# Performance work log

Hardware: AMD Instinct MI355X
Metric: run time of the kernel (lower is better)

## Reference

```python
import jax, jax.numpy as jnp
import numpy as np

HIDDEN = 4096
N_HEADS = 32
HEAD_DIM = HIDDEN // N_HEADS
B = 8
S = 1024
N = B * S


def _build_cos_sin(max_pos, head_dim):
    inv_freq = 1.0 / (10000.0 ** (np.arange(0, head_dim, 2, dtype=np.float32) / head_dim))
    t = np.arange(max_pos, dtype=np.float32)
    freqs = np.outer(t, inv_freq)                 # [max_pos, head_dim/2]
    emb = np.concatenate([freqs, freqs], axis=-1)  # [max_pos, head_dim]
    return jnp.asarray(np.cos(emb)), jnp.asarray(np.sin(emb))


def setup_inputs() -> dict:
    key = jax.random.key(0)
    ks = jax.random.split(key, 5)
    cos, sin = _build_cos_sin(S, HEAD_DIM)
    scale = 0.02
    inp = {
        "cos": cos,
        "sin": sin,
        "nz_hidden_states": jax.random.normal(ks[0], (N, HIDDEN), jnp.float32),
        "nz_position_ids": jnp.tile(jnp.arange(S, dtype=jnp.int32), B),
        "cu_seqlens": jnp.arange(B + 1, dtype=jnp.int32) * S,
        "max_seqlen": S,
        "Wq": jax.random.normal(ks[1], (HIDDEN, HIDDEN), jnp.float32) * scale,
        "Wk": jax.random.normal(ks[2], (HIDDEN, HIDDEN), jnp.float32) * scale,
        "Wv": jax.random.normal(ks[3], (HIDDEN, HIDDEN), jnp.float32) * scale,
        "Wo": jax.random.normal(ks[4], (HIDDEN, HIDDEN), jnp.float32) * scale,
    }
    return inp


def _rotate_half(x):
    x1, x2 = jnp.split(x, 2, axis=-1)
    return jnp.concatenate([-x2, x1], axis=-1)


def reference(cos, sin, nz_hidden_states, nz_position_ids, cu_seqlens, max_seqlen, Wq, Wk, Wv, Wo):
    n_tok = nz_hidden_states.shape[0]
    b = cu_seqlens.shape[0] - 1
    s = n_tok // b  # equal-length packing
    h, d = N_HEADS, HEAD_DIM

    q = (nz_hidden_states @ Wq.T).reshape(n_tok, h, d)
    k = (nz_hidden_states @ Wk.T).reshape(n_tok, h, d)
    v = (nz_hidden_states @ Wv.T).reshape(n_tok, h, d)

    # RoPE: cos/sin gathered per token, broadcast over heads
    c = cos[nz_position_ids][:, None, :]  # [N,1,D]
    sn = sin[nz_position_ids][:, None, :]
    q = q * c + _rotate_half(q) * sn
    k = k * c + _rotate_half(k) * sn

    # Varlen causal attention (equal-length segments -> batch reshape)
    qb = q.reshape(b, s, h, d)
    kb = k.reshape(b, s, h, d)
    vb = v.reshape(b, s, h, d)
    scores = jnp.einsum('bqhd,bkhd->bhqk', qb, kb) / jnp.sqrt(jnp.float32(d))
    causal = jnp.tril(jnp.ones((s, s), dtype=bool))
    scores = jnp.where(causal, scores, jnp.finfo(scores.dtype).min)
    probs = jax.nn.softmax(scores, axis=-1)
    out = jnp.einsum('bhqk,bkhd->bqhd', probs, vb).reshape(n_tok, h * d)
    return out @ Wo.T
```

## Files before the change

kernel.cpp:

```cpp
#include <hip/hip_runtime.h>
#include <hip/hip_bf16.h>

#define NTOK 8192
#define HID 4096
#define NHEADS 32
#define HDIM 128
#define SEQ 1024
#define NSTEP (HID / 32)

typedef float f32x4 __attribute__((ext_vector_type(4)));
typedef short bf16x8 __attribute__((ext_vector_type(8)));

__device__ __forceinline__ ushort f2bf(float f) {
  union { float f; unsigned u; } x;
  x.f = f;
  unsigned r = x.u + 0x7fffu + ((x.u >> 16) & 1u);
  return (ushort)(r >> 16);
}
__device__ __forceinline__ float bf2f(ushort h) {
  union { unsigned u; float f; } x;
  x.u = ((unsigned)h) << 16;
  return x.f;
}

__global__ __launch_bounds__(256) void cvt_bf16_kernel(const float4* __restrict__ in,
                                                       ushort4* __restrict__ out, int n4) {
  int i = blockIdx.x * 256 + threadIdx.x;
  if (i < n4) {
    float4 v = in[i];
    ushort4 o;
    o.x = f2bf(v.x); o.y = f2bf(v.y); o.z = f2bf(v.z); o.w = f2bf(v.w);
    out[i] = o;
  }
}


__device__ __forceinline__ void gload16(const void* g, void* l) {
  __builtin_amdgcn_global_load_lds(
      (const __attribute__((address_space(1))) unsigned int*)g,
      (__attribute__((address_space(3))) unsigned int*)l, 16, 0, 0);
}

__device__ __forceinline__ void stage32(const ushort* gA, const ushort* gB,
                                        int rowA0, int rowB0, int k0,
                                        ushort* ldsA, ushort* ldsB, int tid) {
  const int wid = tid >> 6, lane = tid & 63;
#pragma unroll
  for (int q = 0; q < 2; ++q) {
    int wuni = q * 8192 + wid * 1024;
    int off = wuni + lane * 16;
    int row = off >> 6;
    int kb = (off ^ (((row >> 1) & 3) << 4)) & 63;
    gload16(gA + (size_t)(rowA0 + row) * HID + k0 + (kb >> 1), (char*)ldsA + wuni);
    gload16(gB + (size_t)(rowB0 + row) * HID + k0 + (kb >> 1), (char*)ldsB + wuni);
  }
}

__device__ __forceinline__ void load_frags(const ushort* sA, const ushort* sB,
                                           int wm, int wn, int l15, int l4, int swzr,
                                           bf16x8 af[8], bf16x8 bfr[4]) {
  const char* cA = (const char*)sA;
  const char* cB = (const char*)sB;
#pragma unroll
  for (int ii = 0; ii < 8; ++ii) {
    int L = (wm * 128 + ii * 16 + l15) * 64 + l4 * 16;
    af[ii] = *(const bf16x8*)(cA + (L ^ swzr));
  }
#pragma unroll
  for (int jj = 0; jj < 4; ++jj) {
    int L = (wn * 64 + jj * 16 + l15) * 64 + l4 * 16;
    bfr[jj] = *(const bf16x8*)(cB + (L ^ swzr));
  }
}

#define MFMA_CLUSTER()                                                         \
  do {                                                                         \
    asm volatile("s_waitcnt lgkmcnt(0)" ::: "memory");                         \
    __builtin_amdgcn_sched_barrier(0);                                         \
    __builtin_amdgcn_s_setprio(1);                                             \
    _Pragma("unroll") for (int ii = 0; ii < 8; ++ii)                           \
        _Pragma("unroll") for (int jj = 0; jj < 4; ++jj)                       \
            acc[ii][jj] = __builtin_amdgcn_mfma_f32_16x16x32_bf16(             \
                af[ii], bfr[jj], acc[ii][jj], 0, 0, 0);                        \
    __builtin_amdgcn_s_setprio(0);                                             \
  } while (0)

template <bool OUTF32>
__global__ __launch_bounds__(512, 2) void gemm256_kernel(
    const ushort* __restrict__ Abf,
    const ushort* __restrict__ B0, const ushort* __restrict__ B1,
    const ushort* __restrict__ B2,
    void* __restrict__ O0, void* __restrict__ O1, void* __restrict__ O2,
    int NTALL) {
  __shared__ __align__(16) ushort ringA[4][8192];
  __shared__ __align__(16) ushort ringB[4][8192];

  const int tid = threadIdx.x;
  const int l = tid & 63, wid = tid >> 6;
  const int wm = wid >> 2, wn = wid & 3;
  const int l15 = l & 15, l4 = l >> 4;
  const int swzr = ((l15 >> 1) & 3) << 4;

  const int nwg = gridDim.x;
  const int cpx = nwg >> 3;
  const int bid = blockIdx.x;
  const int lgid = (bid & 7) * cpx + (bid >> 3);
  const int bandw = NTALL << 3;
  const int band = lgid / bandw, rem = lgid % bandw;
  const int nt = rem >> 3;
  const int mt = (band << 3) + (rem & 7);
  const int m0 = mt * 256;
  const int sel = nt >> 4;
  const int n0 = (nt & 15) * 256;
  const ushort* Bp = (sel == 0) ? B0 : ((sel == 1) ? B1 : B2);
  void* Op = (sel == 0) ? O0 : ((sel == 1) ? O1 : O2);

  f32x4 acc[8][4];
  const f32x4 zero = {0.f, 0.f, 0.f, 0.f};
#pragma unroll
  for (int i = 0; i < 8; ++i)
#pragma unroll
    for (int j = 0; j < 4; ++j) acc[i][j] = zero;

  stage32(Abf, Bp, m0, n0, 0, ringA[0], ringB[0], tid);
  stage32(Abf, Bp, m0, n0, 32, ringA[1], ringB[1], tid);
  asm volatile("s_waitcnt vmcnt(4)" ::: "memory");
  __builtin_amdgcn_s_barrier();

  bf16x8 af[8], bfr[4];
#pragma unroll 4
  for (int t = 0; t < NSTEP - 2; ++t) {
    const int slot = t & 3;
    load_frags(ringA[slot], ringB[slot], wm, wn, l15, l4, swzr, af, bfr);
    stage32(Abf, Bp, m0, n0, (t + 2) * 32, ringA[(t + 2) & 3], ringB[(t + 2) & 3], tid);
    MFMA_CLUSTER();
    asm volatile("s_waitcnt vmcnt(4)" ::: "memory");
    __builtin_amdgcn_s_barrier();
  }
  load_frags(ringA[(NSTEP - 2) & 3], ringB[(NSTEP - 2) & 3], wm, wn, l15, l4, swzr, af, bfr);
  MFMA_CLUSTER();
  asm volatile("s_waitcnt vmcnt(0)" ::: "memory");
  __builtin_amdgcn_s_barrier();
  load_frags(ringA[(NSTEP - 1) & 3], ringB[(NSTEP - 1) & 3], wm, wn, l15, l4, swzr, af, bfr);
  MFMA_CLUSTER();

#pragma unroll
  for (int i = 0; i < 8; ++i) {
    const int row = m0 + wm * 128 + i * 16 + l4 * 4;
#pragma unroll
    for (int j = 0; j < 4; ++j) {
      const int col = n0 + wn * 64 + j * 16 + l15;
#pragma unroll
      for (int r = 0; r < 4; ++r) {
        float v = acc[i][j][r];
        if constexpr (OUTF32)
          ((float*)Op)[(size_t)(row + r) * HID + col] = v;
        else
          ((ushort*)Op)[(size_t)(row + r) * HID + col] = f2bf(v);
      }
    }
  }
}

template <bool ISBF>
__device__ __forceinline__ void stage_tile(ushort* lds, const void* gp, int row0, int k0, int tid) {
  if constexpr (ISBF) {
    const ushort* g = (const ushort*)gp;
#pragma unroll
    for (int i = 0; i < 2; ++i) {
      int row = (tid >> 2) + i * 64;
      int gr = tid & 3;
      bf16x8 v = *(const bf16x8*)(g + (size_t)(row0 + row) * HID + k0 + gr * 8);
      int gs = gr ^ ((row >> 1) & 3);
      *(bf16x8*)((char*)lds + row * 64 + gs * 16) = v;
    }
  } else {
    const float* g = (const float*)gp;
    int row = tid >> 1;
    const float* rp = g + (size_t)(row0 + row) * HID + k0;
#pragma unroll
    for (int i = 0; i < 2; ++i) {
      int gr = (tid & 1) * 2 + i;
      float4 a = *(const float4*)(rp + gr * 8);
      float4 b = *(const float4*)(rp + gr * 8 + 4);
      bf16x8 v;
      v[0] = (short)f2bf(a.x); v[1] = (short)f2bf(a.y);
      v[2] = (short)f2bf(a.z); v[3] = (short)f2bf(a.w);
      v[4] = (short)f2bf(b.x); v[5] = (short)f2bf(b.y);
      v[6] = (short)f2bf(b.z); v[7] = (short)f2bf(b.w);
      int gs = gr ^ ((row >> 1) & 3);
      *(bf16x8*)((char*)lds + row * 64 + gs * 16) = v;
    }
  }
}

template <bool ABF, bool BBF, bool OUTF32>
__global__ __launch_bounds__(256) void gemm_bt_kernel(
    const void* __restrict__ Ap,
    const void* __restrict__ B0, const void* __restrict__ B1, const void* __restrict__ B2,
    void* __restrict__ O0, void* __restrict__ O1, void* __restrict__ O2,
    int ntiles_per_w) {
  __shared__ __align__(16) ushort lA[128 * 32];
  __shared__ __align__(16) ushort lB[128 * 32];
  const int tid = threadIdx.x;
  const int l = tid & 63, wid = tid >> 6;
  const int wm = wid >> 1, wn = wid & 1;
  const int l15 = l & 15, l4 = l >> 4;
  const int mt0 = blockIdx.y * 128;
  const int ntile = blockIdx.x;
  const int sel = ntile / ntiles_per_w;
  const int nt0 = (ntile % ntiles_per_w) * 128;
  const void* Bp = (sel == 0) ? B0 : ((sel == 1) ? B1 : B2);
  void* Op = (sel == 0) ? O0 : ((sel == 1) ? O1 : O2);

  const f32x4 zero = {0.f, 0.f, 0.f, 0.f};
  f32x4 acc[4][4];
#pragma unroll
  for (int i = 0; i < 4; ++i)
#pragma unroll
    for (int j = 0; j < 4; ++j) acc[i][j] = zero;

  for (int k0 = 0; k0 < HID; k0 += 32) {
    stage_tile<ABF>(lA, Ap, mt0, k0, tid);
    stage_tile<BBF>(lB, Bp, nt0, k0, tid);
    __syncthreads();
    bf16x8 af[4], bfr[4];
#pragma unroll
    for (int i = 0; i < 4; ++i) {
      int rowa = wm * 64 + i * 16 + l15;
      int ga = l4 ^ ((rowa >> 1) & 3);
      af[i] = *(const bf16x8*)((const char*)lA + rowa * 64 + ga * 16);
      int rowb = wn * 64 + i * 16 + l15;
      int gb = l4 ^ ((rowb >> 1) & 3);
      bfr[i] = *(const bf16x8*)((const char*)lB + rowb * 64 + gb * 16);
    }
#pragma unroll
    for (int i = 0; i < 4; ++i)
#pragma unroll
      for (int j = 0; j < 4; ++j)
        acc[i][j] = __builtin_amdgcn_mfma_f32_16x16x32_bf16(af[i], bfr[j], acc[i][j], 0, 0, 0);
    __syncthreads();
  }

#pragma unroll
  for (int i = 0; i < 4; ++i) {
#pragma unroll
    for (int j = 0; j < 4; ++j) {
      int row = mt0 + wm * 64 + i * 16 + l4 * 4;
      int col = nt0 + wn * 64 + j * 16 + l15;
#pragma unroll
      for (int r = 0; r < 4; ++r) {
        float v = acc[i][j][r];
        if constexpr (OUTF32)
          ((float*)Op)[(size_t)(row + r) * HID + col] = v;
        else
          ((ushort*)Op)[(size_t)(row + r) * HID + col] = f2bf(v);
      }
    }
  }
}

__global__ __launch_bounds__(256) void rope_kernel(
    ushort* __restrict__ q, ushort* __restrict__ k,
    const float* __restrict__ cosT, const float* __restrict__ sinT,
    const int* __restrict__ pos) {
  int idx = blockIdx.x * 256 + threadIdx.x;
  int token = idx >> 8;
  int head = (idx >> 3) & 31;
  int c = idx & 7;
  int p = pos[token];
  size_t base = (size_t)token * HID + head * HDIM + c * 8;
  bf16x8 ql = *(bf16x8*)(q + base);
  bf16x8 qh = *(bf16x8*)(q + base + 64);
  bf16x8 kl = *(bf16x8*)(k + base);
  bf16x8 kh = *(bf16x8*)(k + base + 64);
  float4 c0 = *(const float4*)(cosT + (size_t)p * HDIM + c * 8);
  float4 c1 = *(const float4*)(cosT + (size_t)p * HDIM + c * 8 + 4);
  float4 s0 = *(const float4*)(sinT + (size_t)p * HDIM + c * 8);
  float4 s1 = *(const float4*)(sinT + (size_t)p * HDIM + c * 8 + 4);
  float cs[8] = {c0.x, c0.y, c0.z, c0.w, c1.x, c1.y, c1.z, c1.w};
  float sn[8] = {s0.x, s0.y, s0.z, s0.w, s1.x, s1.y, s1.z, s1.w};
  const float qsc = 0.08838834764831845f;
  bf16x8 qlo, qho, klo, kho;
#pragma unroll
  for (int j = 0; j < 8; ++j) {
    float qlf = bf2f((ushort)ql[j]), qhf = bf2f((ushort)qh[j]);
    float klf = bf2f((ushort)kl[j]), khf = bf2f((ushort)kh[j]);
    qlo[j] = (short)f2bf((qlf * cs[j] - qhf * sn[j]) * qsc);
    qho[j] = (short)f2bf((qhf * cs[j] + qlf * sn[j]) * qsc);
    klo[j] = (short)f2bf(klf * cs[j] - khf * sn[j]);
    kho[j] = (short)f2bf(khf * cs[j] + klf * sn[j]);
  }
  *(bf16x8*)(q + base) = qlo;
  *(bf16x8*)(q + base + 64) = qho;
  *(bf16x8*)(k + base) = klo;
  *(bf16x8*)(k + base + 64) = kho;
}

__global__ __launch_bounds__(256) void attn_kernel(
    const ushort* __restrict__ qb, const ushort* __restrict__ kb,
    const ushort* __restrict__ vb, ushort* __restrict__ ob) {
  __shared__ __align__(16) ushort lK[32 * 128];
  __shared__ __align__(16) ushort lVT[128 * 32];
  __shared__ __align__(16) ushort lP[4][16 * 32];

  const int tid = threadIdx.x;
  const int l = tid & 63, wid = tid >> 6;
  const int l15 = l & 15, l4 = l >> 4;
  const int q0 = blockIdx.x * 64;
  const int h = blockIdx.y;
  const size_t seqbase = (size_t)blockIdx.z * SEQ;

  bf16x8 qf[4];
  {
    const ushort* qp = qb + (seqbase + q0 + wid * 16 + l15) * HID + h * HDIM + l4 * 8;
#pragma unroll
    for (int kk = 0; kk < 4; ++kk) qf[kk] = *(const bf16x8*)(qp + kk * 32);
  }

  const f32x4 zero = {0.f, 0.f, 0.f, 0.f};
  f32x4 oacc[8];
#pragma unroll
  for (int t = 0; t < 8; ++t) oacc[t] = zero;
  float mrow[4] = {-3e38f, -3e38f, -3e38f, -3e38f};
  float lrow[4] = {0.f, 0.f, 0.f, 0.f};

  const int ntile = q0 / 32 + 2;
  for (int kt = 0; kt < ntile; ++kt) {
    const int k0 = kt * 32;
    {
      int r = tid >> 3;
      const ushort* kp = kb + (seqbase + k0 + r) * HID + h * HDIM;
#pragma unroll
      for (int i = 0; i < 2; ++i) {
        int g = (tid & 7) * 2 + i;
        bf16x8 kv = *(const bf16x8*)(kp + g * 8);
        int gs = g ^ (r & 7);
        *(bf16x8*)((char*)lK + r * 256 + gs * 16) = kv;
      }
    }
    {
      int d = tid & 127;
      int j0 = (tid >> 7) * 16;
      const ushort* vp = vb + (seqbase + k0 + j0) * HID + h * HDIM + d;
      ushort tmp[16];
#pragma unroll
      for (int j = 0; j < 16; ++j) tmp[j] = vp[(size_t)j * HID];
#pragma unroll
      for (int i = 0; i < 2; ++i) {
        bf16x8 vv;
#pragma unroll
        for (int jj = 0; jj < 8; ++jj) vv[jj] = (short)tmp[i * 8 + jj];
        int g = (j0 >> 3) + i;
        int gs = g ^ ((d >> 1) & 3);
        *(bf16x8*)((char*)lVT + d * 64 + gs * 16) = vv;
      }
    }
    __syncthreads();

    f32x4 s[2];
#pragma unroll
    for (int hf = 0; hf < 2; ++hf) {
      f32x4 c = zero;
      int row = hf * 16 + l15;
#pragma unroll
      for (int kk = 0; kk < 4; ++kk) {
        int gs = (kk * 4 + l4) ^ (row & 7);
        bf16x8 kf = *(const bf16x8*)((const char*)lK + row * 256 + gs * 16);
        c = __builtin_amdgcn_mfma_f32_16x16x32_bf16(qf[kk], kf, c, 0, 0, 0);
      }
      s[hf] = c;
    }

    const int qrow = q0 + wid * 16 + l4 * 4;
#pragma unroll
    for (int r = 0; r < 4; ++r) {
      float s0 = (k0 + l15 <= qrow + r) ? s[0][r] : -1e30f;
      float s1 = (k0 + 16 + l15 <= qrow + r) ? s[1][r] : -1e30f;
      float tmax = fmaxf(s0, s1);
#pragma unroll
      for (int off = 8; off; off >>= 1) tmax = fmaxf(tmax, __shfl_xor(tmax, off));
      float newm = fmaxf(mrow[r], tmax);
      float sc = __expf(mrow[r] - newm);
      float p0 = __expf(s0 - newm);
      float p1 = __expf(s1 - newm);
      float rs = p0 + p1;
#pragma unroll
      for (int off = 8; off; off >>= 1) rs += __shfl_xor(rs, off);
      lrow[r] = lrow[r] * sc + rs;
      mrow[r] = newm;
#pragma unroll
      for (int t = 0; t < 8; ++t) oacc[t][r] *= sc;
      lP[wid][(l4 * 4 + r) * 32 + l15] = f2bf(p0);
      lP[wid][(l4 * 4 + r) * 32 + 16 + l15] = f2bf(p1);
    }
    asm volatile("s_waitcnt lgkmcnt(0)" ::: "memory");
    __builtin_amdgcn_sched_barrier(0);

    bf16x8 pf = *(const bf16x8*)((const char*)&lP[wid][0] + l15 * 64 + l4 * 16);
#pragma unroll
    for (int t = 0; t < 8; ++t) {
      int d = t * 16 + l15;
      int gs = l4 ^ ((d >> 1) & 3);
      bf16x8 vf = *(const bf16x8*)((const char*)lVT + d * 64 + gs * 16);
      oacc[t] = __builtin_amdgcn_mfma_f32_16x16x32_bf16(pf, vf, oacc[t], 0, 0, 0);
    }
    __syncthreads();
  }

#pragma unroll
  for (int r = 0; r < 4; ++r) {
    float inv = 1.0f / lrow[r];
    ushort* op = ob + (seqbase + q0 + wid * 16 + l4 * 4 + r) * HID + h * HDIM + l15;
#pragma unroll
    for (int t = 0; t < 8; ++t) op[t * 16] = f2bf(oacc[t][r] * inv);
  }
}

extern "C" void kernel_launch(void* const* d_in, const int* in_sizes, int n_in,
                              void* d_out, int out_size, void* d_ws, size_t ws_size,
                              hipStream_t stream) {
  const float* cosT = (const float*)d_in[0];
  const float* sinT = (const float*)d_in[1];
  const float* X    = (const float*)d_in[2];
  const int*   pos  = (const int*)d_in[3];
  const float* Wq = (const float*)d_in[6];
  const float* Wk = (const float*)d_in[7];
  const float* Wv = (const float*)d_in[8];
  const float* Wo = (const float*)d_in[9];
  float* out = (float*)d_out;

  char* ws = (char*)d_ws;
  const size_t QKVB = (size_t)NTOK * HID * 2;
  const size_t WB = (size_t)HID * HID * 2;
  const size_t XB = QKVB;
  ushort* qbuf = (ushort*)(ws);
  ushort* kbuf = (ushort*)(ws + QKVB);
  ushort* vbuf = (ushort*)(ws + 2 * QKVB);

  dim3 blk(256);
  const int n4x = NTOK * HID / 4;
  const int n4w = HID * HID / 4;

  const bool fast = ws_size >= 3 * QKVB + XB + 4 * WB;
  const bool mid = !fast && ws_size >= 3 * QKVB + 2 * WB &&
                   (size_t)out_size * 4 >= XB + 2 * WB;

  if (fast || mid) {
    ushort *xb, *wqb, *wkb, *wvb, *wob;
    if (fast) {
      xb  = (ushort*)(ws + 3 * QKVB);
      wqb = (ushort*)(ws + 3 * QKVB + XB);
      wkb = (ushort*)(ws + 3 * QKVB + XB + WB);
      wvb = (ushort*)(ws + 3 * QKVB + XB + 2 * WB);
      wob = (ushort*)(ws + 3 * QKVB + XB + 3 * WB);
    } else {
      xb  = (ushort*)d_out;
      wqb = (ushort*)((char*)d_out + XB);
      wkb = (ushort*)((char*)d_out + XB + WB);
      wvb = (ushort*)(ws + 3 * QKVB);
      wob = (ushort*)(ws + 3 * QKVB + WB);
    }
    cvt_bf16_kernel<<<n4x / 256, blk, 0, stream>>>((const float4*)X, (ushort4*)xb, n4x);
    cvt_bf16_kernel<<<n4w / 256, blk, 0, stream>>>((const float4*)Wq, (ushort4*)wqb, n4w);
    cvt_bf16_kernel<<<n4w / 256, blk, 0, stream>>>((const float4*)Wk, (ushort4*)wkb, n4w);
    cvt_bf16_kernel<<<n4w / 256, blk, 0, stream>>>((const float4*)Wv, (ushort4*)wvb, n4w);
    cvt_bf16_kernel<<<n4w / 256, blk, 0, stream>>>((const float4*)Wo, (ushort4*)wob, n4w);
    gemm256_kernel<false><<<dim3(32 * 48), dim3(512), 0, stream>>>(
        xb, wqb, wkb, wvb, qbuf, kbuf, vbuf, 48);
    rope_kernel<<<NTOK * NHEADS * 8 / 256, blk, 0, stream>>>(qbuf, kbuf, cosT, sinT, pos);
    attn_kernel<<<dim3(16, 32, 8), blk, 0, stream>>>(qbuf, kbuf, vbuf, qbuf);
    gemm256_kernel<true><<<dim3(32 * 16), dim3(512), 0, stream>>>(
        qbuf, wob, wob, wob, out, out, out, 16);
  } else {
    gemm_bt_kernel<false, false, false><<<dim3(96, 64), blk, 0, stream>>>(
        X, Wq, Wk, Wv, qbuf, kbuf, vbuf, 32);
    rope_kernel<<<NTOK * NHEADS * 8 / 256, blk, 0, stream>>>(qbuf, kbuf, cosT, sinT, pos);
    attn_kernel<<<dim3(16, 32, 8), blk, 0, stream>>>(qbuf, kbuf, vbuf, qbuf);
    gemm_bt_kernel<true, false, true><<<dim3(32, 64), blk, 0, stream>>>(
        qbuf, Wo, Wo, Wo, out, out, out, 32);
  }
}
```

Before: 1.565 ms.

## Double-buffer register fragments and deepen LDS prefetch in GEMM main loop

The GEMM main loop now keeps two sets of register fragments. The LDS fragments for step t+1 are loaded while the MFMAs for step t run, which removes the lgkmcnt(0) wait and sched_barrier that came before each MFMA cluster. Global staging now runs three steps ahead instead of two in the 4-slot ring, and the loop is manually unrolled by four with a hand-written tail. This adds register pressure from the doubled fragment arrays at launch_bounds(512,2), so spills are a risk. The ring-slot reuse and its synchronization are also tighter, because slot t+3 is overwritten while slot t+1 is being read.

```diff
diff --git a/kernel.cpp b/kernel.cpp
--- a/kernel.cpp
+++ b/kernel.cpp
@@ -73,16 +73,22 @@
   }
 }
 
-#define MFMA_CLUSTER()                                                         \
+#define GSTEP(CURA, CURB, NXTA, NXTB, T, DO_STAGE, VMC)                        \
   do {                                                                         \
-    asm volatile("s_waitcnt lgkmcnt(0)" ::: "memory");                         \
-    __builtin_amdgcn_sched_barrier(0);                                         \
     __builtin_amdgcn_s_setprio(1);                                             \
     _Pragma("unroll") for (int ii = 0; ii < 8; ++ii)                           \
         _Pragma("unroll") for (int jj = 0; jj < 4; ++jj)                       \
             acc[ii][jj] = __builtin_amdgcn_mfma_f32_16x16x32_bf16(             \
-                af[ii], bfr[jj], acc[ii][jj], 0, 0, 0);                        \
+                CURA[ii], CURB[jj], acc[ii][jj], 0, 0, 0);                     \
     __builtin_amdgcn_s_setprio(0);                                             \
+    load_frags(ringA[((T) + 1) & 3], ringB[((T) + 1) & 3], wm, wn, l15, l4,    \
+               swzr, NXTA, NXTB);                                              \
+    if (DO_STAGE)                                                              \
+      stage32(Abf, Bp, m0, n0, ((T) + 3) * 32, ringA[((T) + 3) & 3],           \
+              ringB[((T) + 3) & 3], tid);                                      \
+    if ((VMC) == 4) asm volatile("s_waitcnt vmcnt(4)" ::: "memory");           \
+    else if ((VMC) == 0) asm volatile("s_waitcnt vmcnt(0)" ::: "memory");      \
+    __builtin_amdgcn_s_barrier();                                              \
   } while (0)
 
 template <bool OUTF32>
@@ -124,25 +130,43 @@
 
   stage32(Abf, Bp, m0, n0, 0, ringA[0], ringB[0], tid);
   stage32(Abf, Bp, m0, n0, 32, ringA[1], ringB[1], tid);
+  stage32(Abf, Bp, m0, n0, 64, ringA[2], ringB[2], tid);
   asm volatile("s_waitcnt vmcnt(4)" ::: "memory");
   __builtin_amdgcn_s_barrier();
 
-  bf16x8 af[8], bfr[4];
-#pragma unroll 4
-  for (int t = 0; t < NSTEP - 2; ++t) {
-    const int slot = t & 3;
-    load_frags(ringA[slot], ringB[slot], wm, wn, l15, l4, swzr, af, bfr);
-    stage32(Abf, Bp, m0, n0, (t + 2) * 32, ringA[(t + 2) & 3], ringB[(t + 2) & 3], tid);
-    MFMA_CLUSTER();
-    asm volatile("s_waitcnt vmcnt(4)" ::: "memory");
-    __builtin_amdgcn_s_barrier();
-  }
-  load_frags(ringA[(NSTEP - 2) & 3], ringB[(NSTEP - 2) & 3], wm, wn, l15, l4, swzr, af, bfr);
-  MFMA_CLUSTER();
-  asm volatile("s_waitcnt vmcnt(0)" ::: "memory");
-  __builtin_amdgcn_s_barrier();
-  load_frags(ringA[(NSTEP - 1) & 3], ringB[(NSTEP - 1) & 3], wm, wn, l15, l4, swzr, af, bfr);
-  MFMA_CLUSTER();
+  bf16x8 afA[8], bfrA[4], afB[8], bfrB[4];
+  load_frags(ringA[0], ringB[0], wm, wn, l15, l4, swzr, afA, bfrA);
+
+  for (int tt = 0; tt < NSTEP - 4; tt += 4) {
+    GSTEP(afA, bfrA, afB, bfrB, tt + 0, true, 4);
+    GSTEP(afB, bfrB, afA, bfrA, tt + 1, true, 4);
+    GSTEP(afA, bfrA, afB, bfrB, tt + 2, true, 4);
+    GSTEP(afB, bfrB, afA, bfrA, tt + 3, true, 4);
+  }
+  GSTEP(afA, bfrA, afB, bfrB, NSTEP - 4, true, 4);
+  GSTEP(afB, bfrB, afA, bfrA, NSTEP - 3, false, 0);
+  {
+    __builtin_amdgcn_s_setprio(1);
+#pragma unroll
+    for (int ii = 0; ii < 8; ++ii)
+#pragma unroll
+      for (int jj = 0; jj < 4; ++jj)
+        acc[ii][jj] = __builtin_amdgcn_mfma_f32_16x16x32_bf16(
+            afA[ii], bfrA[jj], acc[ii][jj], 0, 0, 0);
+    __builtin_amdgcn_s_setprio(0);
+    load_frags(ringA[(NSTEP - 1) & 3], ringB[(NSTEP - 1) & 3], wm, wn, l15, l4,
+               swzr, afB, bfrB);
+  }
+  {
+    __builtin_amdgcn_s_setprio(1);
+#pragma unroll
+    for (int ii = 0; ii < 8; ++ii)
+#pragma unroll
+      for (int jj = 0; jj < 4; ++jj)
+        acc[ii][jj] = __builtin_amdgcn_mfma_f32_16x16x32_bf16(
+            afB[ii], bfrB[jj], acc[ii][jj], 0, 0, 0);
+    __builtin_amdgcn_s_setprio(0);
+  }
 
 #pragma unroll
   for (int i = 0; i < 8; ++i) {
```

New measurement: 1.718 ms. +9.8%, slower.

## Deepen GEMM prefetch to three stages and split fragment loads into halves

Applied to the files above, without the earlier changes.

The bf16 GEMM main loop now keeps three K-slices in flight in the 4-slot LDS ring instead of two. Each step is split into two half-clusters: it loads 4 A fragments and the B fragments, runs 16 MFMAs, then loads the remaining 4 A fragments for the second 16 MFMAs. This halves the live A-fragment registers and lets LDS reads overlap MFMA work. The loop is manually unrolled by 4 with a hand-written tail. The vmcnt(4) wait still forces the slices two and one step ahead to finish, so the extra prefetch depth may not add much latency hiding, and the extra lgkmcnt waits could stall.

```diff
diff --git a/kernel.cpp b/kernel.cpp
--- a/kernel.cpp
+++ b/kernel.cpp
@@ -56,33 +56,46 @@
   }
 }
 
-__device__ __forceinline__ void load_frags(const ushort* sA, const ushort* sB,
-                                           int wm, int wn, int l15, int l4, int swzr,
-                                           bf16x8 af[8], bf16x8 bfr[4]) {
-  const char* cA = (const char*)sA;
-  const char* cB = (const char*)sB;
-#pragma unroll
-  for (int ii = 0; ii < 8; ++ii) {
-    int L = (wm * 128 + ii * 16 + l15) * 64 + l4 * 16;
-    af[ii] = *(const bf16x8*)(cA + (L ^ swzr));
-  }
-#pragma unroll
-  for (int jj = 0; jj < 4; ++jj) {
-    int L = (wn * 64 + jj * 16 + l15) * 64 + l4 * 16;
-    bfr[jj] = *(const bf16x8*)(cB + (L ^ swzr));
-  }
-}
-
-#define MFMA_CLUSTER()                                                         \
+#define GSTEP(T, DO_STAGE, VMC)                                                \
   do {                                                                         \
+    const char* cA = (const char*)ringA[(T) & 3];                              \
+    const char* cB = (const char*)ringB[(T) & 3];                              \
+                                            \
+    _Pragma("unroll") for (int ii = 0; ii < 4; ++ii) {                         \
+      int L = (wm * 128 + ii * 16 + l15) * 64 + l4 * 16;                       \
+      af[ii] = *(const bf16x8*)(cA + (L ^ swzr));                              \
+    }                                                                          \
+    _Pragma("unroll") for (int jj = 0; jj < 4; ++jj) {                         \
+      int L = (wn * 64 + jj * 16 + l15) * 64 + l4 * 16;                        \
+      bfr[jj] = *(const bf16x8*)(cB + (L ^ swzr));                             \
+    }                                                                          \
+    if (DO_STAGE)                                                              \
+      stage32(Abf, Bp, m0, n0, ((T) + 3) * 32, ringA[((T) + 3) & 3],           \
+              ringB[((T) + 3) & 3], tid);                                      \
     asm volatile("s_waitcnt lgkmcnt(0)" ::: "memory");                         \
     __builtin_amdgcn_sched_barrier(0);                                         \
     __builtin_amdgcn_s_setprio(1);                                             \
-    _Pragma("unroll") for (int ii = 0; ii < 8; ++ii)                           \
+    _Pragma("unroll") for (int ii = 0; ii < 4; ++ii)                           \
         _Pragma("unroll") for (int jj = 0; jj < 4; ++jj)                       \
             acc[ii][jj] = __builtin_amdgcn_mfma_f32_16x16x32_bf16(             \
                 af[ii], bfr[jj], acc[ii][jj], 0, 0, 0);                        \
     __builtin_amdgcn_s_setprio(0);                                             \
+     \
+    _Pragma("unroll") for (int ii = 0; ii < 4; ++ii) {                         \
+      int L = (wm * 128 + (ii + 4) * 16 + l15) * 64 + l4 * 16;                 \
+      af[ii] = *(const bf16x8*)(cA + (L ^ swzr));                              \
+    }                                                                          \
+    asm volatile("s_waitcnt lgkmcnt(0)" ::: "memory");                         \
+    __builtin_amdgcn_sched_barrier(0);                                         \
+    __builtin_amdgcn_s_setprio(1);                                             \
+    _Pragma("unroll") for (int ii = 0; ii < 4; ++ii)                           \
+        _Pragma("unroll") for (int jj = 0; jj < 4; ++jj)                       \
+            acc[ii + 4][jj] = __builtin_amdgcn_mfma_f32_16x16x32_bf16(         \
+                af[ii], bfr[jj], acc[ii + 4][jj], 0, 0, 0);                    \
+    __builtin_amdgcn_s_setprio(0);                                             \
+    if ((VMC) == 4) asm volatile("s_waitcnt vmcnt(4)" ::: "memory");           \
+    else if ((VMC) == 0) asm volatile("s_waitcnt vmcnt(0)" ::: "memory");      \
+    if ((VMC) >= 0) __builtin_amdgcn_s_barrier();                              \
   } while (0)
 
 template <bool OUTF32>
@@ -124,25 +137,21 @@
 
   stage32(Abf, Bp, m0, n0, 0, ringA[0], ringB[0], tid);
   stage32(Abf, Bp, m0, n0, 32, ringA[1], ringB[1], tid);
+  stage32(Abf, Bp, m0, n0, 64, ringA[2], ringB[2], tid);
   asm volatile("s_waitcnt vmcnt(4)" ::: "memory");
   __builtin_amdgcn_s_barrier();
 
-  bf16x8 af[8], bfr[4];
-#pragma unroll 4
-  for (int t = 0; t < NSTEP - 2; ++t) {
-    const int slot = t & 3;
-    load_frags(ringA[slot], ringB[slot], wm, wn, l15, l4, swzr, af, bfr);
-    stage32(Abf, Bp, m0, n0, (t + 2) * 32, ringA[(t + 2) & 3], ringB[(t + 2) & 3], tid);
-    MFMA_CLUSTER();
-    asm volatile("s_waitcnt vmcnt(4)" ::: "memory");
-    __builtin_amdgcn_s_barrier();
-  }
-  load_frags(ringA[(NSTEP - 2) & 3], ringB[(NSTEP - 2) & 3], wm, wn, l15, l4, swzr, af, bfr);
-  MFMA_CLUSTER();
-  asm volatile("s_waitcnt vmcnt(0)" ::: "memory");
-  __builtin_amdgcn_s_barrier();
-  load_frags(ringA[(NSTEP - 1) & 3], ringB[(NSTEP - 1) & 3], wm, wn, l15, l4, swzr, af, bfr);
-  MFMA_CLUSTER();
+  bf16x8 af[4], bfr[4];
+  for (int tt = 0; tt < NSTEP - 4; tt += 4) {
+    GSTEP(tt + 0, true, 4);
+    GSTEP(tt + 1, true, 4);
+    GSTEP(tt + 2, true, 4);
+    GSTEP(tt + 3, true, 4);
+  }
+  GSTEP(NSTEP - 4, true, 4);
+  GSTEP(NSTEP - 3, false, 0);
+  GSTEP(NSTEP - 2, false, -1);
+  GSTEP(NSTEP - 1, false, -1);
 
 #pragma unroll
   for (int i = 0; i < 8; ++i) {
```

Result: no change. 1.545 ms (-1.3%).
